# Kernel tuning notes

Measured on AMD Instinct MI355X. Metric: run time of the kernel, lower is better.

Reference implementation:

```python
import jax, jax.numpy as jnp
import numpy as np
from jax import lax

N_MAX = 350  # fixed adjacency size from the original module

def _conv(x, w, b):
    y = lax.conv_general_dilated(x, w, (1, 1), 'SAME',
                                 dimension_numbers=('NCHW', 'OIHW', 'NCHW'))
    return y + b[None, :, None, None]

def _maxpool2(x):
    return lax.reduce_window(x, -jnp.inf, lax.max, (1, 1, 2, 2), (1, 1, 2, 2), 'VALID')

def _lin(x, w, b):  # torch Linear: w [out,in]
    return x @ w.T + b

def setup_inputs() -> dict:
    key = jax.random.key(0)
    ks = jax.random.split(key, 24)
    B = 16
    images = jax.random.normal(ks[0], (B, 1, 256, 256), dtype=jnp.float32)
    # prefix masks: first n_b nodes valid, n_b in [2, 350]
    counts = jax.random.randint(ks[1], (B,), 2, N_MAX + 1)
    node_masks = jnp.arange(N_MAX)[None, :] < counts[:, None]
    def p(k, shape, s=0.02):
        return jax.random.normal(k, shape, dtype=jnp.float32) * s
    inp = {
        'images': images, 'node_masks': node_masks,
        # baseline CNN: 1->32->64->128->256, 3x3 convs
        'c1w': p(ks[2], (32, 1, 3, 3)),   'c1b': p(ks[3], (32,)),
        'c2w': p(ks[4], (64, 32, 3, 3)),  'c2b': p(ks[5], (64,)),
        'c3w': p(ks[6], (128, 64, 3, 3)), 'c3b': p(ks[7], (128,)),
        'c4w': p(ks[8], (256, 128, 3, 3)),'c4b': p(ks[9], (256,)),
        # node_detector: 256->512->700
        'nd1w': p(ks[10], (512, 256)), 'nd1b': p(ks[11], (512,)),
        'nd2w': p(ks[12], (N_MAX * 2, 512)), 'nd2b': p(ks[13], (N_MAX * 2,)),
        # count_predictor: 256->256->1
        'cp1w': p(ks[14], (256, 256)), 'cp1b': p(ks[15], (256,)),
        'cp2w': p(ks[16], (1, 256)),   'cp2b': p(ks[17], (1,)),
        # mlp_correction: 1->32->16->1
        'mc1w': p(ks[18], (32, 1)),  'mc1b': p(ks[19], (32,)),
        'mc2w': p(ks[20], (16, 32)), 'mc2b': p(ks[21], (16,)),
        'mc3w': p(ks[22], (1, 16)),  'mc3b': p(ks[23], (1,)),
    }
    return inp

def reference(images, node_masks,
              c1w, c1b, c2w, c2b, c3w, c3b, c4w, c4b,
              nd1w, nd1b, nd2w, nd2b,
              cp1w, cp1b, cp2w, cp2b,
              mc1w, mc1b, mc2w, mc2b, mc3w, mc3b):
    B = images.shape[0]
    relu = jax.nn.relu
    # CNN encoder (baseline)
    x = _maxpool2(relu(_conv(images, c1w, c1b)))
    x = _maxpool2(relu(_conv(x, c2w, c2b)))
    x = _maxpool2(relu(_conv(x, c3w, c3b)))
    x = relu(_conv(x, c4w, c4b))
    feat = jnp.mean(x, axis=(2, 3))  # AdaptiveAvgPool2d((1,1)) -> [B,256]
    # node detector (dropout is identity in eval)
    coords = _lin(relu(_lin(feat, nd1w, nd1b)), nd2w, nd2b).reshape(B, N_MAX, 2)
    # count predictor
    count = _lin(relu(_lin(feat, cp1w, cp1b)), cp2w, cp2b)[:, 0]
    # cosine similarity over all 350 slots (row-wise normalize is mask-independent)
    cn = coords / jnp.maximum(jnp.linalg.norm(coords, axis=-1, keepdims=True), 1e-12)
    sim = jnp.einsum('bnd,bmd->bnm', cn, cn)  # [B,350,350]
    # pointwise 1->32->16->1 MLP correction + sigmoid
    h1 = relu(sim[..., None] * mc1w[:, 0] + mc1b)          # [B,N,N,32]
    h2 = relu(jnp.einsum('bnmk,jk->bnmj', h1, mc2w) + mc2b)  # [B,N,N,16]
    corr = jax.nn.sigmoid(jnp.einsum('bnmj,oj->bnmo', h2, mc3w)[..., 0] + mc3b[0])
    # scatter-pad into fixed 350x350: with prefix masks this is elementwise pair masking
    m = node_masks.astype(corr.dtype)
    pair = m[:, :, None] * m[:, None, :]
    valid = (node_masks.sum(-1) > 1).astype(corr.dtype)  # n_nodes<=1 -> zero adj
    adjacency = corr * pair * valid[:, None, None]
    return (coords, adjacency, count)
```

## Files before the change

### kernel.cpp

```cpp
#include <hip/hip_runtime.h>
#include <hip/hip_bf16.h>
#include <math.h>

typedef __hip_bfloat16 bf16;
typedef __attribute__((ext_vector_type(8))) short short8;
typedef __attribute__((ext_vector_type(4))) float f32x4;

__device__ __forceinline__ bf16 f2b(float v){ return __float2bfloat16(v); }
__device__ __forceinline__ float ldf(float v){ return v; }
__device__ __forceinline__ float ldf(bf16 v){ return __bfloat162float(v); }
__device__ __forceinline__ unsigned short fbits(float v){
  __hip_bfloat16 h = __float2bfloat16(v);
  return *reinterpret_cast<unsigned short*>(&h);
}
__device__ __forceinline__ float dot4(float4 a, float4 b){
  return fmaf(a.x,b.x, fmaf(a.y,b.y, fmaf(a.z,b.z, a.w*b.w)));
}
__device__ __forceinline__ void load_lds16(const bf16* src, void* lds){
  __builtin_amdgcn_global_load_lds(
      (const __attribute__((address_space(1))) void*)src,
      (__attribute__((address_space(3))) void*)lds, 16, 0, 0);
}

__global__ __launch_bounds__(256) void k_c1prep(const float* __restrict__ img,
                        const float* __restrict__ c1w, const float* __restrict__ c1b,
                        bf16* __restrict__ x1,
                        const float* __restrict__ c2w, const float* __restrict__ c3w,
                        const float* __restrict__ c4w, bf16* __restrict__ wt2,
                        bf16* __restrict__ wt3, bf16* __restrict__ wt4,
                        const float* __restrict__ w1, const float* __restrict__ b1,
                        const float* __restrict__ w2, const float* __restrict__ b2,
                        const float* __restrict__ w3, const float* __restrict__ b3,
                        float* __restrict__ lut){
  int bid = blockIdx.x;
  int tid = threadIdx.x;
  if(bid >= 1024){
    int pb = bid - 1024;
    if(pb < 1512){
      int e = pb*256 + tid;
      const float* w; bf16* wt; int OC, IC;
      if(e < 18432){ w = c2w; wt = wt2; OC = 64;  IC = 32; }
      else if(e < 92160){ e -= 18432; w = c3w; wt = wt3; OC = 128; IC = 64; }
      else { e -= 92160; w = c4w; wt = wt4; OC = 256; IC = 128; }
      int ic = e % IC; int t2 = e / IC; int oc = t2 % OC; int tap = t2 / OC;
      wt[e] = f2b(w[(oc*IC + ic)*9 + tap]);
    } else {
      int e = (pb-1512)*256 + tid;
      float s = -1.f + (2.f/4095.f)*e;
      float h1[32];
      #pragma unroll
      for(int k=0;k<32;k++) h1[k] = fmaxf(fmaf(s, w1[k], b1[k]), 0.f);
      float a3 = b3[0];
      #pragma unroll
      for(int j=0;j<16;j++){
        float t = b2[j];
        #pragma unroll
        for(int k=0;k<32;k++) t = fmaf(h1[k], w2[j*32+k], t);
        a3 = fmaf(fmaxf(t,0.f), w3[j], a3);
      }
      lut[e] = 1.f/(1.f + expf(-a3));
    }
    return;
  }
  __shared__ float Wl[288], Bl[32];
  for(int t=tid; t<288; t+=256) Wl[t] = c1w[t];
  if(tid<32) Bl[tid] = c1b[tid];
  __syncthreads();
  int idx = bid*256 + tid;
  int ox = idx & 127, oy = (idx>>7)&127, b = idx>>14;
  const float4* ip4 = (const float4*)(img + (size_t)b*65536);
  int y0 = oy*2-1;
  int a  = (2*ox - 1) >> 2;
  bool odd = (ox & 1);
  float patch[4][4];
  #pragma unroll
  for(int py=0;py<4;py++){
    int y = y0+py; bool yok = (unsigned)y<256u;
    float4 A = make_float4(0.f,0.f,0.f,0.f), B = make_float4(0.f,0.f,0.f,0.f);
    if(yok && a >= 0) A = ip4[y*64 + a];
    if(yok && a < 63) B = ip4[y*64 + a + 1];
    patch[py][0] = odd ? A.y : A.w;
    patch[py][1] = odd ? A.z : B.x;
    patch[py][2] = odd ? A.w : B.y;
    patch[py][3] = odd ? B.x : B.z;
  }
  unsigned u[16];
  #pragma unroll
  for(int og=0; og<16; og++){
    unsigned short hb[2];
    #pragma unroll
    for(int h=0; h<2; h++){
      int oc = og*2 + h;
      const float* wj = &Wl[oc*9];
      float best = 0.f;
      #pragma unroll
      for(int py=0;py<2;py++)
      #pragma unroll
      for(int px=0;px<2;px++){
        float a2 = Bl[oc];
        #pragma unroll
        for(int ky=0;ky<3;ky++)
        #pragma unroll
        for(int kx=0;kx<3;kx++)
          a2 = fmaf(wj[ky*3+kx], patch[py+ky][px+kx], a2);
        best = fmaxf(best, a2);
      }
      hb[h] = fbits(best);
    }
    u[og] = (unsigned)hb[0] | ((unsigned)hb[1] << 16);
  }
  uint4* dst = (uint4*)(x1 + (size_t)idx*32);
  dst[0] = make_uint4(u[0],u[1],u[2],u[3]);
  dst[1] = make_uint4(u[4],u[5],u[6],u[7]);
  dst[2] = make_uint4(u[8],u[9],u[10],u[11]);
  dst[3] = make_uint4(u[12],u[13],u[14],u[15]);
}

template<int L>
__global__ __launch_bounds__(256) void k_convmfma(const bf16* __restrict__ in,
                      const bf16* __restrict__ wt, const float* __restrict__ bias,
                      bf16* __restrict__ out, float* __restrict__ partial2){
  constexpr int IC   = L==2?32:(L==3?64:128);
  constexpr int OC   = L==2?64:(L==3?128:256);
  constexpr int HW   = L==2?128:(L==3?64:32);
  constexpr int POOL = L==4?0:1;
  constexpr int WNF  = L==4?2:4;
  constexpr int IC8  = IC/8;
  constexpr int SM   = (IC8-1)&7;
  constexpr int KC   = IC/32;
  constexpr int XT   = HW;
  constexpr int ROW  = XT*IC8;
  constexpr int ROWC = (XT+2)*IC8;
  __shared__ short8 T[4*ROWC];

  int bid = blockIdx.x;
  int b, py, bt = 0;
  if(L==4){ b = bid>>5; py = (bid>>1)&15; bt = bid&1; }
  else if(L==3){ b = bid>>5; py = bid&31; }
  else { b = bid>>6; py = bid&63; }

  int tid = threadIdx.x;
  int w = tid>>6, l15 = tid&15, lhi = (tid>>4)&3, lane = tid&63;

  int mbase, nbase;
  if(L==2){ mbase = w*32; nbase = 0; }
  else if(L==3){ mbase = (w&1)*32; nbase = (w>>1)*64; }
  else { mbase = 0; nbase = bt*128 + w*32; }

  for(int c=tid; c<4*2*IC8; c+=256){
    int r = c/(2*IC8), rem = c%(2*IC8);
    int X = (rem>=IC8)?(XT+1):0;
    int k = rem%IC8;
    short8 z = {0,0,0,0,0,0,0,0};
    T[(r*(XT+2)+X)*IC8 + k] = z;
  }
  for(int c0=0; c0<4*ROW; c0+=256){
    int cw  = c0 + w*64;
    int r   = cw / ROW;
    int rem = cw % ROW;
    int gy  = 2*py - 1 + r;
    int ldsbase = (r*(XT+2)+1)*IC8 + rem;
    if((unsigned)gy < (unsigned)HW){
      int remL = rem + lane;
      int x = remL / IC8, k = remL % IC8;
      int ksrc = k ^ ((x+1)&SM);
      const bf16* src = in + (((size_t)b*HW + gy)*XT + x)*IC + ksrc*8;
      load_lds16(src, (void*)&T[ldsbase]);
    } else {
      short8 z = {0,0,0,0,0,0,0,0};
      T[ldsbase + lane] = z;
    }
  }
  __syncthreads();

  float bv[WNF];
  #pragma unroll
  for(int n=0;n<WNF;n++) bv[n] = bias[nbase + n*16 + l15];
  f32x4 acc[2][2][WNF];
  #pragma unroll
  for(int r=0;r<2;r++)
  #pragma unroll
  for(int m=0;m<2;m++)
  #pragma unroll
  for(int n=0;n<WNF;n++){
    acc[r][m][n][0]=bv[n]; acc[r][m][n][1]=bv[n];
    acc[r][m][n][2]=bv[n]; acc[r][m][n][3]=bv[n];
  }

  const short8* wt8 = (const short8*)wt;
  #pragma unroll
  for(int tap=0; tap<9; tap++){
    const int dy = tap/3 - 1, dx = tap%3 - 1;
    #pragma unroll
    for(int kc=0; kc<KC; kc++){
      short8 Bf[WNF];
      #pragma unroll
      for(int n=0;n<WNF;n++){
        int oc = nbase + n*16 + l15;
        Bf[n] = wt8[(size_t)(tap*OC + oc)*IC8 + kc*4 + lhi];
      }
      short8 Af[2][2];
      #pragma unroll
      for(int r=0;r<2;r++)
      #pragma unroll
      for(int m=0;m<2;m++){
        int X = mbase + m*16 + l15 + dx + 1;
        int rs = r + dy + 1;
        Af[r][m] = T[(rs*(XT+2)+X)*IC8 + ((kc*4+lhi) ^ (X&SM))];
      }
      __builtin_amdgcn_s_setprio(1);
      #pragma unroll
      for(int r=0;r<2;r++)
      #pragma unroll
      for(int m=0;m<2;m++)
      #pragma unroll
      for(int n=0;n<WNF;n++)
        acc[r][m][n] = __builtin_amdgcn_mfma_f32_16x16x32_bf16(Af[r][m], Bf[n], acc[r][m][n], 0,0,0);
      __builtin_amdgcn_s_setprio(0);
    }
  }

  if(POOL){
    constexpr int HP = HW/2;
    #pragma unroll
    for(int m=0;m<2;m++)
    #pragma unroll
    for(int n=0;n<WNF;n++){
      int oc = nbase + n*16 + l15;
      #pragma unroll
      for(int t=0;t<2;t++){
        float v = fmaxf(fmaxf(acc[0][m][n][2*t], acc[0][m][n][2*t+1]),
                        fmaxf(acc[1][m][n][2*t], acc[1][m][n][2*t+1]));
        v = fmaxf(v, 0.f);
        int xp = (mbase + m*16)/2 + lhi*2 + t;
        out[(((size_t)b*HP + py)*HP + xp)*OC + oc] = f2b(v);
      }
    }
  } else {
    #pragma unroll
    for(int n=0;n<WNF;n++){
      float p = 0.f;
      #pragma unroll
      for(int r=0;r<2;r++)
      #pragma unroll
      for(int m=0;m<2;m++)
      #pragma unroll
      for(int j=0;j<4;j++)
        p += fmaxf(acc[r][m][n][j], 0.f);
      p += __shfl_xor(p, 16);
      p += __shfl_xor(p, 32);
      if(lhi == 0)
        partial2[((size_t)(b*16+py))*256 + nbase + n*16 + l15] = p;
    }
  }
}

__global__ __launch_bounds__(256) void k_headA(const float* __restrict__ partial2,
                      const float* __restrict__ nd1w, const float* __restrict__ nd1b,
                      const float* __restrict__ cp1w, const float* __restrict__ cp1b,
                      float* __restrict__ h512, float* __restrict__ h256){
  __shared__ float F[256];
  int b = blockIdx.x / 192, blk = blockIdx.x % 192;
  int tid = threadIdx.x;
  float s = 0.f;
  #pragma unroll
  for(int q=0;q<16;q++) s += partial2[((size_t)(b*16+q))*256 + tid];
  F[tid] = s * (1.f/1024.f);
  __syncthreads();
  int w = tid>>6, lane = tid&63;
  int o = blk*4 + w;
  float4 xv = ((const float4*)F)[lane];
  const float* wrow; float bb; float* dst; int oo;
  if(o < 512){ wrow = nd1w + (size_t)o*256; bb = nd1b[o]; dst = h512 + b*512 + o; }
  else { oo = o - 512; wrow = cp1w + (size_t)oo*256; bb = cp1b[oo]; dst = h256 + b*256 + oo; }
  float a = dot4(((const float4*)wrow)[lane], xv);
  #pragma unroll
  for(int off=32; off>0; off>>=1) a += __shfl_xor(a, off);
  if(lane==0) *dst = fmaxf(a + bb, 0.f);
}

__device__ __forceinline__ int mask_mode(const void* p){
  unsigned w0 = ((const unsigned*)p)[0];
  unsigned w1 = ((const unsigned*)p)[1];
  if(w0 == 1u) return (w1 == 0u) ? 4 : 0;
  if(w0 == 0x3F800000u) return 3;
  unsigned short h0 = (unsigned short)(w0 & 0xFFFFu);
  if(h0 == 0x3F80u || h0 == 0x3C00u) return 2;
  return 1;
}
__device__ __forceinline__ int mask_get(const void* p, int i, int mode){
  switch(mode){
    case 0: return ((const int*)p)[i] != 0;
    case 1: return ((const unsigned char*)p)[i] != 0;
    case 2: return ((const unsigned short*)p)[i] != 0;
    case 3: return ((const float*)p)[i] != 0.f;
    default: return ((const long long*)p)[i] != 0ll;
  }
}

__global__ __launch_bounds__(256) void k_headB(const float* __restrict__ h512,
                      const float* __restrict__ h256,
                      const float* __restrict__ nd2w, const float* __restrict__ nd2b,
                      const float* __restrict__ cp2w, const float* __restrict__ cp2b,
                      const void* __restrict__ masks,
                      float* __restrict__ coordsOut, float* __restrict__ countOut,
                      int* __restrict__ counts){
  int b = blockIdx.x / 176, blk = blockIdx.x % 176;
  int tid = threadIdx.x;
  int w = tid>>6, lane = tid&63;
  int o = blk*4 + w;
  if(o == 701){
    int mode = mask_mode(masks);
    int c = 0;
    for(int i=lane; i<350; i+=64) c += mask_get(masks, b*350+i, mode);
    #pragma unroll
    for(int off=32; off>0; off>>=1) c += __shfl_xor(c, off);
    if(lane==0) counts[b] = c;
    return;
  }
  if(o > 700) return;
  float a;
  if(o < 700){
    const float4* xp = (const float4*)(h512 + b*512);
    const float4* wp = (const float4*)(nd2w + (size_t)o*512);
    a = dot4(wp[lane], xp[lane]) + dot4(wp[lane+64], xp[lane+64]);
  } else {
    const float4* xp = (const float4*)(h256 + b*256);
    const float4* wp = (const float4*)cp2w;
    a = dot4(wp[lane], xp[lane]);
  }
  #pragma unroll
  for(int off=32; off>0; off>>=1) a += __shfl_xor(a, off);
  if(lane==0){
    if(o < 700) coordsOut[b*700 + o] = a + nd2b[o];
    else        countOut[b] = a + cp2b[0];
  }
}

__global__ __launch_bounds__(256) void k_adj(const float* __restrict__ coords,
                      const int* __restrict__ counts, const float* __restrict__ lut,
                      float* __restrict__ out){
  int t4 = blockIdx.x*256 + threadIdx.x;
  if(t4 >= 490000) return;
  int base = t4*4;
  int b = base / 122500;
  int rem = base % 122500;
  int cnt = counts[b];
  int valid = cnt > 1;
  float res[4];
  #pragma unroll
  for(int e=0;e<4;e++){
    int n = (rem+e)/350, m = (rem+e)%350;
    float o = 0.f;
    if(valid && n < cnt && m < cnt){
      float2 a = ((const float2*)coords)[b*350+n];
      float2 c = ((const float2*)coords)[b*350+m];
      float nn = fmaxf(fmaf(a.x,a.x, a.y*a.y), 1e-24f);
      float mm = fmaxf(fmaf(c.x,c.x, c.y*c.y), 1e-24f);
      float s = fmaf(a.x, c.x, a.y*c.y) * __frsqrt_rn(nn) * __frsqrt_rn(mm);
      float u = (s + 1.f) * 2047.5f;
      u = fminf(fmaxf(u, 0.f), 4095.f);
      int i = min((int)u, 4094);
      float fr = u - (float)i;
      float l0 = lut[i], l1 = lut[i+1];
      o = fmaf(l1 - l0, fr, l0);
    }
    res[e] = o;
  }
  *(float4*)(out + base) = make_float4(res[0], res[1], res[2], res[3]);
}

extern "C" void kernel_launch(void* const* d_in, const int* in_sizes, int n_in,
                              void* d_out, int out_size, void* d_ws, size_t ws_size,
                              hipStream_t stream){
  const float* images = (const float*)d_in[0];
  const void*  masks  = d_in[1];
  const float *c1w=(const float*)d_in[2],  *c1b=(const float*)d_in[3];
  const float *c2w=(const float*)d_in[4],  *c2b=(const float*)d_in[5];
  const float *c3w=(const float*)d_in[6],  *c3b=(const float*)d_in[7];
  const float *c4w=(const float*)d_in[8],  *c4b=(const float*)d_in[9];
  const float *nd1w=(const float*)d_in[10],*nd1b=(const float*)d_in[11];
  const float *nd2w=(const float*)d_in[12],*nd2b=(const float*)d_in[13];
  const float *cp1w=(const float*)d_in[14],*cp1b=(const float*)d_in[15];
  const float *cp2w=(const float*)d_in[16],*cp2b=(const float*)d_in[17];
  const float *mc1w=(const float*)d_in[18],*mc1b=(const float*)d_in[19];
  const float *mc2w=(const float*)d_in[20],*mc2b=(const float*)d_in[21];
  const float *mc3w=(const float*)d_in[22],*mc3b=(const float*)d_in[23];
  float* out = (float*)d_out;

  char* W = (char*)d_ws;
  float* partial2 = (float*)W;
  float* h512     = (float*)(W + 262144);
  float* h256     = (float*)(W + 294912);
  float* lut      = (float*)(W + 311296);
  int*   counts   = (int*)(W + 327680);
  bf16*  wt2 = (bf16*)(W + 524288);
  bf16*  wt3 = (bf16*)(W + 589824);
  bf16*  wt4 = (bf16*)(W + 786432);
  bf16*  x1 = (bf16*)(W + 2097152);
  bf16*  x2 = (bf16*)(W + 2097152 + 16777216);
  bf16*  x3 = (bf16*)(W + 2097152);

  float* coordsOut = out;
  float* adjOut    = out + 11200;
  float* countOut  = out + 11200 + 1960000;

  k_c1prep<<<2552, 256, 0, stream>>>(images, c1w, c1b, x1,
                                     c2w, c3w, c4w, wt2, wt3, wt4,
                                     mc1w, mc1b, mc2w, mc2b, mc3w, mc3b, lut);
  k_convmfma<2><<<1024, 256, 0, stream>>>(x1, wt2, c2b, x2, nullptr);
  k_convmfma<3><<<512, 256, 0, stream>>>(x2, wt3, c3b, x3, nullptr);
  k_convmfma<4><<<512, 256, 0, stream>>>(x3, wt4, c4b, nullptr, partial2);
  k_headA<<<3072, 256, 0, stream>>>(partial2, nd1w, nd1b, cp1w, cp1b, h512, h256);
  k_headB<<<2816, 256, 0, stream>>>(h512, h256, nd2w, nd2b, cp2w, cp2b, masks,
                                    coordsOut, countOut, counts);
  k_adj<<<1915, 256, 0, stream>>>(coordsOut, counts, lut, adjOut);
}
```

Measured before the change: 92.67 us.

## Merge head and adjacency tail kernels into one cooperative grid-synced kernel

Replaces the three separate head-A, head-B and adjacency kernels with one persistent cooperative kernel of 1024 blocks. The kernel loops over the old block indices and uses grid-wide syncs between phases. This is meant to remove kernel launch gaps and drain/fill overhead between the small tail stages. In exchange it adds cooperative launch and grid barrier costs, and it caps parallelism at 1024 resident blocks.

```diff
diff --git a/kernel.cpp b/kernel.cpp
--- a/kernel.cpp
+++ b/kernel.cpp
@@ -1,6 +1,9 @@
 #include <hip/hip_runtime.h>
+#include <hip/hip_cooperative_groups.h>
 #include <hip/hip_bf16.h>
 #include <math.h>
+
+namespace cg = cooperative_groups;
 
 typedef __hip_bfloat16 bf16;
 typedef __attribute__((ext_vector_type(8))) short short8;
@@ -20,6 +23,25 @@
   __builtin_amdgcn_global_load_lds(
       (const __attribute__((address_space(1))) void*)src,
       (__attribute__((address_space(3))) void*)lds, 16, 0, 0);
+}
+
+__device__ __forceinline__ int mask_mode(const void* p){
+  unsigned w0 = ((const unsigned*)p)[0];
+  unsigned w1 = ((const unsigned*)p)[1];
+  if(w0 == 1u) return (w1 == 0u) ? 4 : 0;
+  if(w0 == 0x3F800000u) return 3;
+  unsigned short h0 = (unsigned short)(w0 & 0xFFFFu);
+  if(h0 == 0x3F80u || h0 == 0x3C00u) return 2;
+  return 1;
+}
+__device__ __forceinline__ int mask_get(const void* p, int i, int mode){
+  switch(mode){
+    case 0: return ((const int*)p)[i] != 0;
+    case 1: return ((const unsigned char*)p)[i] != 0;
+    case 2: return ((const unsigned short*)p)[i] != 0;
+    case 3: return ((const float*)p)[i] != 0.f;
+    default: return ((const long long*)p)[i] != 0ll;
+  }
 }
 
 __global__ __launch_bounds__(256) void k_c1prep(const float* __restrict__ img,
@@ -255,119 +277,103 @@
   }
 }
 
-__global__ __launch_bounds__(256) void k_headA(const float* __restrict__ partial2,
-                      const float* __restrict__ nd1w, const float* __restrict__ nd1b,
-                      const float* __restrict__ cp1w, const float* __restrict__ cp1b,
-                      float* __restrict__ h512, float* __restrict__ h256){
+__global__ __launch_bounds__(256, 4) void k_tail(
+    const float* __restrict__ partial2, const void* __restrict__ masks,
+    const float* __restrict__ nd1w, const float* __restrict__ nd1b,
+    const float* __restrict__ cp1w, const float* __restrict__ cp1b,
+    const float* __restrict__ nd2w, const float* __restrict__ nd2b,
+    const float* __restrict__ cp2w, const float* __restrict__ cp2b,
+    const float* __restrict__ lut,
+    float* __restrict__ h512, float* __restrict__ h256,
+    float* __restrict__ coordsOut, float* __restrict__ countOut,
+    int* __restrict__ counts){
+  cg::grid_group grid = cg::this_grid();
   __shared__ float F[256];
-  int b = blockIdx.x / 192, blk = blockIdx.x % 192;
-  int tid = threadIdx.x;
-  float s = 0.f;
-  #pragma unroll
-  for(int q=0;q<16;q++) s += partial2[((size_t)(b*16+q))*256 + tid];
-  F[tid] = s * (1.f/1024.f);
-  __syncthreads();
-  int w = tid>>6, lane = tid&63;
-  int o = blk*4 + w;
-  float4 xv = ((const float4*)F)[lane];
-  const float* wrow; float bb; float* dst; int oo;
-  if(o < 512){ wrow = nd1w + (size_t)o*256; bb = nd1b[o]; dst = h512 + b*512 + o; }
-  else { oo = o - 512; wrow = cp1w + (size_t)oo*256; bb = cp1b[oo]; dst = h256 + b*256 + oo; }
-  float a = dot4(((const float4*)wrow)[lane], xv);
-  #pragma unroll
-  for(int off=32; off>0; off>>=1) a += __shfl_xor(a, off);
-  if(lane==0) *dst = fmaxf(a + bb, 0.f);
-}
-
-__device__ __forceinline__ int mask_mode(const void* p){
-  unsigned w0 = ((const unsigned*)p)[0];
-  unsigned w1 = ((const unsigned*)p)[1];
-  if(w0 == 1u) return (w1 == 0u) ? 4 : 0;
-  if(w0 == 0x3F800000u) return 3;
-  unsigned short h0 = (unsigned short)(w0 & 0xFFFFu);
-  if(h0 == 0x3F80u || h0 == 0x3C00u) return 2;
-  return 1;
-}
-__device__ __forceinline__ int mask_get(const void* p, int i, int mode){
-  switch(mode){
-    case 0: return ((const int*)p)[i] != 0;
-    case 1: return ((const unsigned char*)p)[i] != 0;
-    case 2: return ((const unsigned short*)p)[i] != 0;
-    case 3: return ((const float*)p)[i] != 0.f;
-    default: return ((const long long*)p)[i] != 0ll;
-  }
-}
-
-__global__ __launch_bounds__(256) void k_headB(const float* __restrict__ h512,
-                      const float* __restrict__ h256,
-                      const float* __restrict__ nd2w, const float* __restrict__ nd2b,
-                      const float* __restrict__ cp2w, const float* __restrict__ cp2b,
-                      const void* __restrict__ masks,
-                      float* __restrict__ coordsOut, float* __restrict__ countOut,
-                      int* __restrict__ counts){
-  int b = blockIdx.x / 176, blk = blockIdx.x % 176;
   int tid = threadIdx.x;
   int w = tid>>6, lane = tid&63;
-  int o = blk*4 + w;
-  if(o == 701){
-    int mode = mask_mode(masks);
-    int c = 0;
-    for(int i=lane; i<350; i+=64) c += mask_get(masks, b*350+i, mode);
-    #pragma unroll
-    for(int off=32; off>0; off>>=1) c += __shfl_xor(c, off);
-    if(lane==0) counts[b] = c;
-    return;
-  }
-  if(o > 700) return;
-  float a;
-  if(o < 700){
-    const float4* xp = (const float4*)(h512 + b*512);
-    const float4* wp = (const float4*)(nd2w + (size_t)o*512);
-    a = dot4(wp[lane], xp[lane]) + dot4(wp[lane+64], xp[lane+64]);
-  } else {
-    const float4* xp = (const float4*)(h256 + b*256);
-    const float4* wp = (const float4*)cp2w;
-    a = dot4(wp[lane], xp[lane]);
-  }
-  #pragma unroll
-  for(int off=32; off>0; off>>=1) a += __shfl_xor(a, off);
-  if(lane==0){
-    if(o < 700) coordsOut[b*700 + o] = a + nd2b[o];
-    else        countOut[b] = a + cp2b[0];
-  }
-}
-
-__global__ __launch_bounds__(256) void k_adj(const float* __restrict__ coords,
-                      const int* __restrict__ counts, const float* __restrict__ lut,
-                      float* __restrict__ out){
-  int t4 = blockIdx.x*256 + threadIdx.x;
-  if(t4 >= 490000) return;
-  int base = t4*4;
-  int b = base / 122500;
-  int rem = base % 122500;
-  int cnt = counts[b];
-  int valid = cnt > 1;
-  float res[4];
-  #pragma unroll
-  for(int e=0;e<4;e++){
-    int n = (rem+e)/350, m = (rem+e)%350;
-    float o = 0.f;
-    if(valid && n < cnt && m < cnt){
-      float2 a = ((const float2*)coords)[b*350+n];
-      float2 c = ((const float2*)coords)[b*350+m];
-      float nn = fmaxf(fmaf(a.x,a.x, a.y*a.y), 1e-24f);
-      float mm = fmaxf(fmaf(c.x,c.x, c.y*c.y), 1e-24f);
-      float s = fmaf(a.x, c.x, a.y*c.y) * __frsqrt_rn(nn) * __frsqrt_rn(mm);
-      float u = (s + 1.f) * 2047.5f;
-      u = fminf(fmaxf(u, 0.f), 4095.f);
-      int i = min((int)u, 4094);
-      float fr = u - (float)i;
-      float l0 = lut[i], l1 = lut[i+1];
-      o = fmaf(l1 - l0, fr, l0);
-    }
-    res[e] = o;
-  }
-  *(float4*)(out + base) = make_float4(res[0], res[1], res[2], res[3]);
+
+  for(int u = blockIdx.x; u < 3072; u += 1024){
+    int b = u / 192, blk = u % 192;
+    float s = 0.f;
+    #pragma unroll
+    for(int q=0;q<16;q++) s += partial2[((size_t)(b*16+q))*256 + tid];
+    F[tid] = s * (1.f/1024.f);
+    __syncthreads();
+    int o = blk*4 + w;
+    float4 xv = ((const float4*)F)[lane];
+    const float* wrow; float bb; float* dst; int oo;
+    if(o < 512){ wrow = nd1w + (size_t)o*256; bb = nd1b[o]; dst = h512 + b*512 + o; }
+    else { oo = o - 512; wrow = cp1w + (size_t)oo*256; bb = cp1b[oo]; dst = h256 + b*256 + oo; }
+    float a = dot4(((const float4*)wrow)[lane], xv);
+    #pragma unroll
+    for(int off=32; off>0; off>>=1) a += __shfl_xor(a, off);
+    if(lane==0) *dst = fmaxf(a + bb, 0.f);
+    __syncthreads();
+  }
+  grid.sync();
+
+  for(int u = blockIdx.x; u < 2816; u += 1024){
+    int b = u / 176, blk = u % 176;
+    int o = blk*4 + w;
+    if(o == 701){
+      int mode = mask_mode(masks);
+      int c = 0;
+      for(int i=lane; i<350; i+=64) c += mask_get(masks, b*350+i, mode);
+      #pragma unroll
+      for(int off=32; off>0; off>>=1) c += __shfl_xor(c, off);
+      if(lane==0) counts[b] = c;
+      continue;
+    }
+    if(o > 700) continue;
+    float a;
+    if(o < 700){
+      const float4* xp = (const float4*)(h512 + b*512);
+      const float4* wp = (const float4*)(nd2w + (size_t)o*512);
+      a = dot4(wp[lane], xp[lane]) + dot4(wp[lane+64], xp[lane+64]);
+    } else {
+      const float4* xp = (const float4*)(h256 + b*256);
+      const float4* wp = (const float4*)cp2w;
+      a = dot4(wp[lane], xp[lane]);
+    }
+    #pragma unroll
+    for(int off=32; off>0; off>>=1) a += __shfl_xor(a, off);
+    if(lane==0){
+      if(o < 700) coordsOut[b*700 + o] = a + nd2b[o];
+      else        countOut[b] = a + cp2b[0];
+    }
+  }
+  grid.sync();
+
+  for(int u = blockIdx.x; u < 1915; u += 1024){
+    int t4 = u*256 + tid;
+    if(t4 >= 490000) continue;
+    int base = t4*4;
+    int b = base / 122500;
+    int rem = base % 122500;
+    int cnt = counts[b];
+    int valid = cnt > 1;
+    float res[4];
+    #pragma unroll
+    for(int e=0;e<4;e++){
+      int n = (rem+e)/350, m = (rem+e)%350;
+      float o = 0.f;
+      if(valid && n < cnt && m < cnt){
+        float2 a = ((const float2*)coordsOut)[b*350+n];
+        float2 c = ((const float2*)coordsOut)[b*350+m];
+        float nn = fmaxf(fmaf(a.x,a.x, a.y*a.y), 1e-24f);
+        float mm = fmaxf(fmaf(c.x,c.x, c.y*c.y), 1e-24f);
+        float s = fmaf(a.x, c.x, a.y*c.y) * __frsqrt_rn(nn) * __frsqrt_rn(mm);
+        float uu = (s + 1.f) * 2047.5f;
+        uu = fminf(fmaxf(uu, 0.f), 4095.f);
+        int i = min((int)uu, 4094);
+        float fr = uu - (float)i;
+        float l0 = lut[i], l1 = lut[i+1];
+        o = fmaf(l1 - l0, fr, l0);
+      }
+      res[e] = o;
+    }
+    *(float4*)(coordsOut + 11200 + base) = make_float4(res[0], res[1], res[2], res[3]);
+  }
 }
 
 extern "C" void kernel_launch(void* const* d_in, const int* in_sizes, int n_in,
@@ -402,7 +408,6 @@
   bf16*  x3 = (bf16*)(W + 2097152);
 
   float* coordsOut = out;
-  float* adjOut    = out + 11200;
   float* countOut  = out + 11200 + 1960000;
 
   k_c1prep<<<2552, 256, 0, stream>>>(images, c1w, c1b, x1,
@@ -411,8 +416,14 @@
   k_convmfma<2><<<1024, 256, 0, stream>>>(x1, wt2, c2b, x2, nullptr);
   k_convmfma<3><<<512, 256, 0, stream>>>(x2, wt3, c3b, x3, nullptr);
   k_convmfma<4><<<512, 256, 0, stream>>>(x3, wt4, c4b, nullptr, partial2);
-  k_headA<<<3072, 256, 0, stream>>>(partial2, nd1w, nd1b, cp1w, cp1b, h512, h256);
-  k_headB<<<2816, 256, 0, stream>>>(h512, h256, nd2w, nd2b, cp2w, cp2b, masks,
-                                    coordsOut, countOut, counts);
-  k_adj<<<1915, 256, 0, stream>>>(coordsOut, counts, lut, adjOut);
-}
+
+  void* args[] = {
+    (void*)&partial2, (void*)&masks,
+    (void*)&nd1w, (void*)&nd1b, (void*)&cp1w, (void*)&cp1b,
+    (void*)&nd2w, (void*)&nd2b, (void*)&cp2w, (void*)&cp2b,
+    (void*)&lut, (void*)&h512, (void*)&h256,
+    (void*)&coordsOut, (void*)&countOut, (void*)&counts
+  };
+  hipLaunchCooperativeKernel((const void*)k_tail, dim3(1024), dim3(256),
+                             args, 0, stream);
+}
```

Result: slower. 267.2 us (+188.3%).
